# Optimization experiments

Measured on AMD Instinct MI355X. Metric: run time of the kernel, lower is better.

The kernel has to match this reference:

```python
import jax, jax.numpy as jnp
import numpy as np

B, C, E = 4, 2048, 1024
H, D = 16, 64


def setup_inputs() -> dict:
    key = jax.random.key(0)
    kx, kq, kk, kv, ko = jax.random.split(key, 5)
    s = 0.02
    return {
        "x": jax.random.normal(kx, (B, C, E), dtype=jnp.float32),
        "W_q": jax.random.normal(kq, (E, H * D), dtype=jnp.float32) * s,
        "W_k": jax.random.normal(kk, (E, H * D), dtype=jnp.float32) * s,
        "W_v": jax.random.normal(kv, (E, H * D), dtype=jnp.float32) * s,
        "W_o": jax.random.normal(ko, (H * D, E), dtype=jnp.float32) * s,
    }


def reference(x, W_q, W_k, W_v, W_o):
    b, c, e = x.shape
    # projections -> [B, H, C, D]
    def split_heads(t):
        return t.reshape(b, c, H, D).transpose(0, 2, 1, 3)
    Q = split_heads(x @ W_q)
    K = split_heads(x @ W_k)
    V = split_heads(x @ W_v)
    scale = 1.0 / jnp.sqrt(jnp.asarray(D, dtype=x.dtype))
    scores = jnp.einsum("bhqd,bhkd->bhqk", Q, K) * scale  # [B,H,C,C]
    causal = jnp.tril(jnp.ones((c, c), dtype=bool))
    scores = jnp.where(causal, scores, jnp.asarray(-jnp.inf, dtype=scores.dtype))
    weights = jax.nn.softmax(scores, axis=-1)
    hidden = jnp.einsum("bhqk,bhkd->bhqd", weights, V)  # [B,H,C,D]
    hidden = hidden.transpose(0, 2, 1, 3).reshape(b, c, H * D)
    return hidden @ W_o
```

## Files before the change

kernel.cpp:

```cpp
#include <hip/hip_runtime.h>

typedef __bf16 bf16;
typedef __attribute__((ext_vector_type(8))) __bf16 bf16x8;
typedef __attribute__((ext_vector_type(4))) __bf16 bf16x4;
typedef __attribute__((ext_vector_type(4))) float f32x4;
typedef __attribute__((ext_vector_type(16))) float f32x16;

#define B_ 4
#define C_ 2048
#define E_ 1024
#define H_ 16
#define D_ 64

__device__ __forceinline__ void gload16(const void* g, void* l) {
  __builtin_amdgcn_global_load_lds(
      (const __attribute__((address_space(1))) void*)g,
      (__attribute__((address_space(3))) void*)l, 16, 0, 0);
}

__device__ __forceinline__ unsigned cvtpk(float lo, float hi) {
  unsigned r;
  asm("v_cvt_pk_bf16_f32 %0, %1, %2" : "=v"(r) : "v"(lo), "v"(hi));
  return r;
}
__device__ __forceinline__ void pswap(unsigned& a, unsigned& b) {
  asm volatile("v_permlane32_swap_b32 %0, %1" : "+v"(a), "+v"(b));
}
__device__ __forceinline__ bf16x8 mkfrag(unsigned d0, unsigned d1, unsigned d2,
                                         unsigned d3) {
  union {
    unsigned u[4];
    bf16x8 v;
  } x;
  x.u[0] = d0;
  x.u[1] = d1;
  x.u[2] = d2;
  x.u[3] = d3;
  return x.v;
}

__global__ __launch_bounds__(256) void xconv(const float* __restrict__ x,
                                             bf16* __restrict__ xb) {
  const size_t i = (size_t)blockIdx.x * 256 + threadIdx.x;
  const float4* p = (const float4*)(x + i * 8);
  float4 a = p[0], b = p[1];
  bf16x8 v = {(__bf16)a.x, (__bf16)a.y, (__bf16)a.z, (__bf16)a.w,
              (__bf16)b.x, (__bf16)b.y, (__bf16)b.z, (__bf16)b.w};
  *(bf16x8*)(xb + i * 8) = v;
}

__global__ __launch_bounds__(256) void wtrans(const float* __restrict__ Wq,
                                              const float* __restrict__ Wk,
                                              const float* __restrict__ Wv,
                                              const float* __restrict__ Wo,
                                              bf16* __restrict__ WT) {
  const float* W = blockIdx.z == 0 ? Wq : blockIdx.z == 1 ? Wk
                 : blockIdx.z == 2 ? Wv : Wo;
  bf16* dst = WT + (size_t)blockIdx.z * 1024 * 1024;
  __shared__ bf16 t[64][65];
  const int tx = threadIdx.x & 63, ty = threadIdx.x >> 6;
  const int r0 = blockIdx.y * 64, c0 = blockIdx.x * 64;
#pragma unroll
  for (int r = ty; r < 64; r += 4)
    t[tx][r] = (__bf16)W[(size_t)(r0 + r) * 1024 + c0 + tx];
  __syncthreads();
#pragma unroll
  for (int r = ty; r < 64; r += 4)
    dst[(size_t)(c0 + r) * 1024 + r0 + tx] = t[r][tx];
}

template <int MODE>
__global__ __launch_bounds__(256, 2) void gemm_bt(const bf16* __restrict__ A,
                                                  const bf16* __restrict__ WTall,
                                                  bf16* __restrict__ Qo,
                                                  bf16* __restrict__ Ko,
                                                  bf16* __restrict__ Vto,
                                                  float* __restrict__ Fo) {
  constexpr int BK = 64;
  constexpr int NT = 1024 / BK;
  const int tid = threadIdx.x;
  const int wave = tid >> 6, lane = tid & 63;
  const int cl = lane & 15, g = lane >> 4;
  const int wr = wave >> 1, wc = wave & 1;
  const int brow = blockIdx.x * 128;
  const int bcol = blockIdx.y * 128;
  const bf16* Bt =
      (MODE == 0) ? (WTall + (size_t)blockIdx.z * 1024 * 1024) : WTall;

  __shared__ __align__(16) bf16 ldsA[2][128 * BK];
  __shared__ __align__(16) bf16 ldsB[2][128 * BK];

  f32x4 acc[4][4] = {};

  auto STAGE = [&](int kt, int buf) {
#pragma unroll
    for (int it = 0; it < 4; ++it) {
      const int chunk = it * 256 + tid;
      const int row = chunk >> 3, slot = chunk & 7;
      const int se = (slot ^ (row & 7)) * 8;
      const int ldsoff = (it * 256 + wave * 64) * 16;
      gload16(A + (size_t)(brow + row) * 1024 + kt + se,
              (char*)&ldsA[buf][0] + ldsoff);
      gload16(Bt + (size_t)(bcol + row) * 1024 + kt + se,
              (char*)&ldsB[buf][0] + ldsoff);
    }
  };

  STAGE(0, 0);
  STAGE(BK, 1);
  asm volatile("s_waitcnt vmcnt(8)" ::: "memory");
  __builtin_amdgcn_s_barrier();

  for (int t = 0; t < NT; ++t) {
    const int buf = t & 1;
    bf16x8 af[2][4], bfr[2][4];
#pragma unroll
    for (int kkid = 0; kkid < 2; ++kkid) {
#pragma unroll
      for (int i = 0; i < 4; ++i) {
        const int sl = ((4 * kkid + g) ^ (cl & 7)) * 8;
        af[kkid][i] = *(const bf16x8*)&ldsA[buf][(wr * 64 + i * 16 + cl) * BK + sl];
        bfr[kkid][i] = *(const bf16x8*)&ldsB[buf][(wc * 64 + i * 16 + cl) * BK + sl];
      }
    }
    asm volatile("s_waitcnt lgkmcnt(0)" ::: "memory");
    __builtin_amdgcn_sched_barrier(0);
    __builtin_amdgcn_s_barrier();

    if (t + 2 < NT) STAGE((t + 2) * BK, buf);

#pragma unroll
    for (int kkid = 0; kkid < 2; ++kkid)
#pragma unroll
      for (int i = 0; i < 4; ++i)
#pragma unroll
        for (int j = 0; j < 4; ++j)
          acc[i][j] = __builtin_amdgcn_mfma_f32_16x16x32_bf16(
              af[kkid][i], bfr[kkid][j], acc[i][j], 0, 0, 0);

    if (t + 2 < NT)
      asm volatile("s_waitcnt vmcnt(8)" ::: "memory");
    else
      asm volatile("s_waitcnt vmcnt(0)" ::: "memory");
    __builtin_amdgcn_s_barrier();
  }

  bf16* dst = nullptr;
  if constexpr (MODE == 0)
    dst = blockIdx.z == 0 ? Qo : blockIdx.z == 1 ? Ko : Vto;
  const float presc =
      (MODE == 0 && blockIdx.z == 0) ? 0.18033688011112042f : 1.0f;
#pragma unroll
  for (int i = 0; i < 4; ++i) {
#pragma unroll
    for (int j = 0; j < 4; ++j) {
#pragma unroll
      for (int r = 0; r < 4; ++r) {
        const int gr = brow + wr * 64 + i * 16 + g * 4 + r;
        const int gc = bcol + wc * 64 + j * 16 + cl;
        const float v = acc[i][j][r] * presc;
        if constexpr (MODE == 0) {
          const int b = gr >> 11, c = gr & 2047;
          const int h = gc >> 6, d = gc & 63;
          if (blockIdx.z == 2)
            dst[(((size_t)b * H_ + h) * D_ + d) * C_ + c] = (__bf16)v;
          else
            dst[(((size_t)b * H_ + h) * C_ + c) * D_ + d] = (__bf16)v;
        } else {
          Fo[(size_t)gr * 1024 + gc] = v;
        }
      }
    }
  }
}

__device__ __forceinline__ void sm_fixed(f32x16& s0, f32x16& s1, f32x4& l4,
                                         int th0, bool domask, int hi,
                                         bf16x8& pf0, bf16x8& pf1,
                                         bf16x8& pf2, bf16x8& pf3) {
  if (domask) {
#pragma unroll
    for (int r = 0; r < 16; ++r) {
      const int crow = (r & 3) + 8 * (r >> 2) + 4 * hi;
      if (crow > th0) s0[r] = -1e30f;
      if (crow + 32 > th0) s1[r] = -1e30f;
    }
  }
#pragma unroll
  for (int r = 0; r < 16; ++r) {
    s0[r] = __builtin_amdgcn_exp2f(s0[r]);
    s1[r] = __builtin_amdgcn_exp2f(s1[r]);
  }
#pragma unroll
  for (int r = 0; r < 16; ++r) l4[r & 3] += s0[r] + s1[r];
  unsigned a0 = cvtpk(s0[0], s0[1]), a1 = cvtpk(s0[2], s0[3]);
  unsigned b0 = cvtpk(s0[4], s0[5]), b1 = cvtpk(s0[6], s0[7]);
  unsigned c0 = cvtpk(s0[8], s0[9]), c1 = cvtpk(s0[10], s0[11]);
  unsigned d0 = cvtpk(s0[12], s0[13]), d1 = cvtpk(s0[14], s0[15]);
  unsigned e0 = cvtpk(s1[0], s1[1]), e1 = cvtpk(s1[2], s1[3]);
  unsigned f0 = cvtpk(s1[4], s1[5]), f1 = cvtpk(s1[6], s1[7]);
  unsigned g0 = cvtpk(s1[8], s1[9]), g1 = cvtpk(s1[10], s1[11]);
  unsigned h0 = cvtpk(s1[12], s1[13]), h1 = cvtpk(s1[14], s1[15]);
  pswap(a0, b0);
  pswap(a1, b1);
  pswap(c0, d0);
  pswap(c1, d1);
  pswap(e0, f0);
  pswap(e1, f1);
  pswap(g0, h0);
  pswap(g1, h1);
  pf0 = mkfrag(a0, a1, b0, b1);
  pf1 = mkfrag(c0, c1, d0, d1);
  pf2 = mkfrag(e0, e1, f0, f1);
  pf3 = mkfrag(g0, g1, h0, h1);
}

__global__ __launch_bounds__(256, 2) void attn(const bf16* __restrict__ Qg,
                                               const bf16* __restrict__ Kg,
                                               const bf16* __restrict__ Vt,
                                               bf16* __restrict__ Hid) {
  const int tid = threadIdx.x, wave = tid >> 6, lane = tid & 63;
  const int l31 = lane & 31, hi = lane >> 5, l7 = lane & 7;
  const int qa = blockIdx.x, qb = 15 - (int)blockIdx.x;
  const int h = blockIdx.y, b = blockIdx.z;
  const size_t bh = (size_t)b * H_ + h;

  __shared__ __align__(16) bf16 ldsK[2 * 64 * 64];
  __shared__ __align__(16) bf16 ldsV[2 * 64 * 64];

  const bf16* Kb = Kg + bh * C_ * D_;
  const bf16* Vb = Vt + bh * (size_t)D_ * C_;

  const int qrowA = qa * 128 + wave * 32;
  const int qrowB = qb * 128 + wave * 32;

  bf16x8 qfA[4], qfB[4];
  {
    const bf16* qra = Qg + (bh * C_ + qrowA + l31) * D_;
    const bf16* qrb = Qg + (bh * C_ + qrowB + l31) * D_;
#pragma unroll
    for (int ds = 0; ds < 4; ++ds) {
      qfA[ds] = *(const bf16x8*)(qra + ds * 16 + 8 * hi);
      qfB[ds] = *(const bf16x8*)(qrb + ds * 16 + 8 * hi);
    }
  }

  f32x4 l4A = {}, l4B = {};
  f32x16 oA0 = {}, oA1 = {}, oB0 = {}, oB1 = {};

  auto STAGE = [&](int kt, int buf) {
#pragma unroll
    for (int it = 0; it < 2; ++it) {
      const int chunk = it * 256 + tid;
      const int row = chunk >> 3, slot = chunk & 7;
      const int se = (slot ^ (row & 7)) * 8;
      const int ldsoff = buf * 8192 + (it * 256 + wave * 64) * 16;
      gload16(Kb + (size_t)kt * 64 * D_ + row * 64 + se, (char*)ldsK + ldsoff);
      gload16(Vb + (size_t)row * C_ + kt * 64 + se, (char*)ldsV + ldsoff);
    }
  };

  const int last = 2 * qb + 1;
  STAGE(0, 0);

  for (int kt = 0; kt <= last; ++kt) {
    const int cur = kt & 1;
    const bf16* kb = ldsK + cur * 4096;
    const bf16* vb = ldsV + cur * 4096;
    if (kt < last) {
      STAGE(kt + 1, cur ^ 1);
      asm volatile("s_waitcnt vmcnt(4)" ::: "memory");
    } else {
      asm volatile("s_waitcnt vmcnt(0)" ::: "memory");
    }
    __builtin_amdgcn_s_barrier();
    __builtin_amdgcn_sched_barrier(0);

    const bool actA = (kt * 64 <= qrowA + 31);
    const bool actB = (kt * 64 <= qrowB + 31);

    f32x16 sA0 = {}, sA1 = {}, sB0 = {}, sB1 = {};
    __builtin_amdgcn_s_setprio(1);
#pragma unroll
    for (int ds = 0; ds < 4; ++ds) {
      const int sl = ((2 * ds + hi) ^ l7) * 8;
      bf16x8 kf0 = *(const bf16x8*)&kb[l31 * 64 + sl];
      bf16x8 kf1 = *(const bf16x8*)&kb[(32 + l31) * 64 + sl];
      if (actA) {
        sA0 = __builtin_amdgcn_mfma_f32_32x32x16_bf16(kf0, qfA[ds], sA0, 0, 0, 0);
        sA1 = __builtin_amdgcn_mfma_f32_32x32x16_bf16(kf1, qfA[ds], sA1, 0, 0, 0);
      }
      if (actB) {
        sB0 = __builtin_amdgcn_mfma_f32_32x32x16_bf16(kf0, qfB[ds], sB0, 0, 0, 0);
        sB1 = __builtin_amdgcn_mfma_f32_32x32x16_bf16(kf1, qfB[ds], sB1, 0, 0, 0);
      }
    }
    __builtin_amdgcn_s_setprio(0);

    bf16x8 vf0[4], vf1[4];
#pragma unroll
    for (int ks = 0; ks < 4; ++ks) {
      const int sl = ((2 * ks + hi) ^ l7) * 8;
      vf0[ks] = *(const bf16x8*)&vb[l31 * 64 + sl];
      vf1[ks] = *(const bf16x8*)&vb[(32 + l31) * 64 + sl];
    }

    if (actA) {
      bf16x8 p0, p1, p2, p3;
      sm_fixed(sA0, sA1, l4A, qrowA + l31 - kt * 64, kt * 64 + 63 > qrowA, hi,
               p0, p1, p2, p3);
      __builtin_amdgcn_s_setprio(1);
      oA0 = __builtin_amdgcn_mfma_f32_32x32x16_bf16(vf0[0], p0, oA0, 0, 0, 0);
      oA1 = __builtin_amdgcn_mfma_f32_32x32x16_bf16(vf1[0], p0, oA1, 0, 0, 0);
      oA0 = __builtin_amdgcn_mfma_f32_32x32x16_bf16(vf0[1], p1, oA0, 0, 0, 0);
      oA1 = __builtin_amdgcn_mfma_f32_32x32x16_bf16(vf1[1], p1, oA1, 0, 0, 0);
      oA0 = __builtin_amdgcn_mfma_f32_32x32x16_bf16(vf0[2], p2, oA0, 0, 0, 0);
      oA1 = __builtin_amdgcn_mfma_f32_32x32x16_bf16(vf1[2], p2, oA1, 0, 0, 0);
      oA0 = __builtin_amdgcn_mfma_f32_32x32x16_bf16(vf0[3], p3, oA0, 0, 0, 0);
      oA1 = __builtin_amdgcn_mfma_f32_32x32x16_bf16(vf1[3], p3, oA1, 0, 0, 0);
      __builtin_amdgcn_s_setprio(0);
    }
    if (actB) {
      bf16x8 p0, p1, p2, p3;
      sm_fixed(sB0, sB1, l4B, qrowB + l31 - kt * 64, kt * 64 + 63 > qrowB, hi,
               p0, p1, p2, p3);
      __builtin_amdgcn_s_setprio(1);
      oB0 = __builtin_amdgcn_mfma_f32_32x32x16_bf16(vf0[0], p0, oB0, 0, 0, 0);
      oB1 = __builtin_amdgcn_mfma_f32_32x32x16_bf16(vf1[0], p0, oB1, 0, 0, 0);
      oB0 = __builtin_amdgcn_mfma_f32_32x32x16_bf16(vf0[1], p1, oB0, 0, 0, 0);
      oB1 = __builtin_amdgcn_mfma_f32_32x32x16_bf16(vf1[1], p1, oB1, 0, 0, 0);
      oB0 = __builtin_amdgcn_mfma_f32_32x32x16_bf16(vf0[2], p2, oB0, 0, 0, 0);
      oB1 = __builtin_amdgcn_mfma_f32_32x32x16_bf16(vf1[2], p2, oB1, 0, 0, 0);
      oB0 = __builtin_amdgcn_mfma_f32_32x32x16_bf16(vf0[3], p3, oB0, 0, 0, 0);
      oB1 = __builtin_amdgcn_mfma_f32_32x32x16_bf16(vf1[3], p3, oB1, 0, 0, 0);
      __builtin_amdgcn_s_setprio(0);
    }
    __builtin_amdgcn_s_barrier();
  }

#pragma unroll
  for (int st = 0; st < 2; ++st) {
    const f32x4 l4 = st ? l4B : l4A;
    float l = (l4[0] + l4[1]) + (l4[2] + l4[3]);
    l += __shfl_xor(l, 32, 64);
    const float inv = 1.0f / l;
    const int qrow = st ? qrowB : qrowA;
    const size_t row = (size_t)b * C_ + qrow + l31;
#pragma unroll
    for (int dt = 0; dt < 2; ++dt) {
      const f32x16& oo = st ? (dt ? oB1 : oB0) : (dt ? oA1 : oA0);
#pragma unroll
      for (int q4 = 0; q4 < 4; ++q4) {
        bf16x4 pk = {(__bf16)(oo[4 * q4 + 0] * inv),
                     (__bf16)(oo[4 * q4 + 1] * inv),
                     (__bf16)(oo[4 * q4 + 2] * inv),
                     (__bf16)(oo[4 * q4 + 3] * inv)};
        const int d = dt * 32 + 8 * q4 + 4 * hi;
        *(bf16x4*)&Hid[row * (H_ * D_) + h * 64 + d] = pk;
      }
    }
  }
}

extern "C" void kernel_launch(void* const* d_in, const int* in_sizes, int n_in,
                              void* d_out, int out_size, void* d_ws,
                              size_t ws_size, hipStream_t stream) {
  const float* x = (const float*)d_in[0];
  const float* Wq = (const float*)d_in[1];
  const float* Wk = (const float*)d_in[2];
  const float* Wv = (const float*)d_in[3];
  const float* Wo = (const float*)d_in[4];

  char* ws = (char*)d_ws;
  bf16* xb = (bf16*)ws;
  bf16* WT = (bf16*)(ws + (16ull << 20));
  bf16* Qb = (bf16*)(ws + (24ull << 20));
  bf16* Kb = (bf16*)(ws + (40ull << 20));
  bf16* Vtb = (bf16*)(ws + (56ull << 20));
  bf16* Hid = (bf16*)(ws + (72ull << 20));

  xconv<<<dim3(4096), 256, 0, stream>>>(x, xb);
  wtrans<<<dim3(16, 16, 4), 256, 0, stream>>>(Wq, Wk, Wv, Wo, WT);
  gemm_bt<0><<<dim3(64, 8, 3), 256, 0, stream>>>(xb, WT, Qb, Kb, Vtb, nullptr);
  attn<<<dim3(8, H_, B_), 256, 0, stream>>>(Qb, Kb, Vtb, Hid);
  gemm_bt<1><<<dim3(64, 8, 1), 256, 0, stream>>>(
      Hid, WT + 3ull * 1024 * 1024, nullptr, nullptr, nullptr, (float*)d_out);
}
```

Baseline: 160.4 us.

## Fuse x fp32-to-bf16 conversion into QKV GEMM and widen attention KV tiles

Removes the separate xconv kernel: the QKV projection GEMM now loads fp32 x into registers, converts it to bf16 with packed converts, and writes it swizzled into LDS, with the waitcnt pipeline restructured around this. It also raises MFMA priority around the GEMM compute loop. The attention kernel stages 128-key K/V tiles per iteration, processed as two 64-key halves, which halves the number of barriers and staging rounds but doubles LDS use. The GEMM reads twice as many bytes of x per tile and relies on register staging instead of direct global-to-LDS loads, and the larger attention LDS footprint may lower occupancy.

```diff
diff --git a/kernel.cpp b/kernel.cpp
--- a/kernel.cpp
+++ b/kernel.cpp
@@ -39,16 +39,6 @@
   return x.v;
 }
 
-__global__ __launch_bounds__(256) void xconv(const float* __restrict__ x,
-                                             bf16* __restrict__ xb) {
-  const size_t i = (size_t)blockIdx.x * 256 + threadIdx.x;
-  const float4* p = (const float4*)(x + i * 8);
-  float4 a = p[0], b = p[1];
-  bf16x8 v = {(__bf16)a.x, (__bf16)a.y, (__bf16)a.z, (__bf16)a.w,
-              (__bf16)b.x, (__bf16)b.y, (__bf16)b.z, (__bf16)b.w};
-  *(bf16x8*)(xb + i * 8) = v;
-}
-
 __global__ __launch_bounds__(256) void wtrans(const float* __restrict__ Wq,
                                               const float* __restrict__ Wk,
                                               const float* __restrict__ Wv,
@@ -70,7 +60,8 @@
 }
 
 template <int MODE>
-__global__ __launch_bounds__(256, 2) void gemm_bt(const bf16* __restrict__ A,
+__global__ __launch_bounds__(256, 2) void gemm_bt(const float* __restrict__ X,
+                                                  const bf16* __restrict__ Ahid,
                                                   const bf16* __restrict__ WTall,
                                                   bf16* __restrict__ Qo,
                                                   bf16* __restrict__ Ko,
@@ -91,25 +82,70 @@
   __shared__ __align__(16) bf16 ldsB[2][128 * BK];
 
   f32x4 acc[4][4] = {};
-
-  auto STAGE = [&](int kt, int buf) {
+  float4 ar[8];
+
+  auto ISSUE_B = [&](int kt, int buf) {
 #pragma unroll
     for (int it = 0; it < 4; ++it) {
       const int chunk = it * 256 + tid;
       const int row = chunk >> 3, slot = chunk & 7;
       const int se = (slot ^ (row & 7)) * 8;
-      const int ldsoff = (it * 256 + wave * 64) * 16;
-      gload16(A + (size_t)(brow + row) * 1024 + kt + se,
-              (char*)&ldsA[buf][0] + ldsoff);
       gload16(Bt + (size_t)(bcol + row) * 1024 + kt + se,
-              (char*)&ldsB[buf][0] + ldsoff);
+              (char*)&ldsB[buf][0] + (it * 256 + wave * 64) * 16);
     }
   };
-
-  STAGE(0, 0);
-  STAGE(BK, 1);
-  asm volatile("s_waitcnt vmcnt(8)" ::: "memory");
-  __builtin_amdgcn_s_barrier();
+  auto ISSUE_A = [&](int kt, int buf) {
+    if constexpr (MODE == 0) {
+#pragma unroll
+      for (int w = 0; w < 4; ++w) {
+        const int chunk = w * 256 + tid;
+        const int row = chunk >> 3, slot = chunk & 7;
+        const float* src = X + (size_t)(brow + row) * 1024 + kt + slot * 8;
+        ar[2 * w] = *(const float4*)(src);
+        ar[2 * w + 1] = *(const float4*)(src + 4);
+      }
+    } else {
+#pragma unroll
+      for (int it = 0; it < 4; ++it) {
+        const int chunk = it * 256 + tid;
+        const int row = chunk >> 3, slot = chunk & 7;
+        const int se = (slot ^ (row & 7)) * 8;
+        gload16(Ahid + (size_t)(brow + row) * 1024 + kt + se,
+                (char*)&ldsA[buf][0] + (it * 256 + wave * 64) * 16);
+      }
+    }
+  };
+  auto WRITE_A = [&](int buf) {
+#pragma unroll
+    for (int w = 0; w < 4; ++w) {
+      const int chunk = w * 256 + tid;
+      const int row = chunk >> 3, slot = chunk & 7;
+      const unsigned p0 = cvtpk(ar[2 * w].x, ar[2 * w].y);
+      const unsigned p1 = cvtpk(ar[2 * w].z, ar[2 * w].w);
+      const unsigned p2 = cvtpk(ar[2 * w + 1].x, ar[2 * w + 1].y);
+      const unsigned p3 = cvtpk(ar[2 * w + 1].z, ar[2 * w + 1].w);
+      *(bf16x8*)((char*)&ldsA[buf][0] + row * 128 + ((slot ^ (row & 7)) * 16)) =
+          mkfrag(p0, p1, p2, p3);
+    }
+  };
+
+  if constexpr (MODE == 0) {
+    ISSUE_A(0, 0);
+    ISSUE_B(0, 0);
+    asm volatile("s_waitcnt vmcnt(0)" ::: "memory");
+    WRITE_A(0);
+    ISSUE_A(BK, 1);
+    ISSUE_B(BK, 1);
+    asm volatile("s_waitcnt lgkmcnt(0)" ::: "memory");
+    __builtin_amdgcn_s_barrier();
+  } else {
+    ISSUE_A(0, 0);
+    ISSUE_B(0, 0);
+    ISSUE_A(BK, 1);
+    ISSUE_B(BK, 1);
+    asm volatile("s_waitcnt vmcnt(8)" ::: "memory");
+    __builtin_amdgcn_s_barrier();
+  }
 
   for (int t = 0; t < NT; ++t) {
     const int buf = t & 1;
@@ -127,8 +163,24 @@
     __builtin_amdgcn_sched_barrier(0);
     __builtin_amdgcn_s_barrier();
 
-    if (t + 2 < NT) STAGE((t + 2) * BK, buf);
-
+    if constexpr (MODE == 0) {
+      if (t + 1 < NT) {
+        asm volatile("s_waitcnt vmcnt(4)" ::: "memory");
+        WRITE_A(buf ^ 1);
+      }
+      if (t + 2 < NT) {
+        ISSUE_A((t + 2) * BK, buf);
+        ISSUE_B((t + 2) * BK, buf);
+      }
+      __builtin_amdgcn_sched_barrier(0);
+    } else {
+      if (t + 2 < NT) {
+        ISSUE_A((t + 2) * BK, buf);
+        ISSUE_B((t + 2) * BK, buf);
+      }
+    }
+
+    __builtin_amdgcn_s_setprio(1);
 #pragma unroll
     for (int kkid = 0; kkid < 2; ++kkid)
 #pragma unroll
@@ -137,11 +189,21 @@
         for (int j = 0; j < 4; ++j)
           acc[i][j] = __builtin_amdgcn_mfma_f32_16x16x32_bf16(
               af[kkid][i], bfr[kkid][j], acc[i][j], 0, 0, 0);
-
-    if (t + 2 < NT)
-      asm volatile("s_waitcnt vmcnt(8)" ::: "memory");
-    else
-      asm volatile("s_waitcnt vmcnt(0)" ::: "memory");
+    __builtin_amdgcn_s_setprio(0);
+
+    if constexpr (MODE == 0) {
+      if (t + 2 < NT)
+        asm volatile("s_waitcnt vmcnt(12)" ::: "memory");
+      else if (t + 1 < NT)
+        asm volatile("s_waitcnt vmcnt(0)" ::: "memory");
+      if (t + 1 < NT)
+        asm volatile("s_waitcnt lgkmcnt(0)" ::: "memory");
+    } else {
+      if (t + 2 < NT)
+        asm volatile("s_waitcnt vmcnt(8)" ::: "memory");
+      else
+        asm volatile("s_waitcnt vmcnt(0)" ::: "memory");
+    }
     __builtin_amdgcn_s_barrier();
   }
 
@@ -225,8 +287,8 @@
   const int h = blockIdx.y, b = blockIdx.z;
   const size_t bh = (size_t)b * H_ + h;
 
-  __shared__ __align__(16) bf16 ldsK[2 * 64 * 64];
-  __shared__ __align__(16) bf16 ldsV[2 * 64 * 64];
+  __shared__ __align__(16) bf16 ldsK[2 * 128 * 64];
+  __shared__ __align__(16) bf16 ldsV[2 * 64 * 128];
 
   const bf16* Kb = Kg + bh * C_ * D_;
   const bf16* Vb = Vt + bh * (size_t)D_ * C_;
@@ -250,90 +312,102 @@
 
   auto STAGE = [&](int kt, int buf) {
 #pragma unroll
-    for (int it = 0; it < 2; ++it) {
-      const int chunk = it * 256 + tid;
-      const int row = chunk >> 3, slot = chunk & 7;
-      const int se = (slot ^ (row & 7)) * 8;
-      const int ldsoff = buf * 8192 + (it * 256 + wave * 64) * 16;
-      gload16(Kb + (size_t)kt * 64 * D_ + row * 64 + se, (char*)ldsK + ldsoff);
-      gload16(Vb + (size_t)row * C_ + kt * 64 + se, (char*)ldsV + ldsoff);
+    for (int w = 0; w < 4; ++w) {
+      const int chunk = w * 256 + tid;
+      {
+        const int row = chunk >> 3, slot = chunk & 7;
+        const int se = (slot ^ (row & 7)) * 8;
+        gload16(Kb + ((size_t)kt * 128 + row) * D_ + se,
+                (char*)ldsK + buf * 16384 + (w * 256 + wave * 64) * 16);
+      }
+      {
+        const int row = chunk >> 4, slot = chunk & 15;
+        const int se = (slot ^ (row & 7)) * 8;
+        gload16(Vb + (size_t)row * C_ + kt * 128 + se,
+                (char*)ldsV + buf * 16384 + (w * 256 + wave * 64) * 16);
+      }
     }
   };
 
-  const int last = 2 * qb + 1;
+  const int nkv = qb + 1;
   STAGE(0, 0);
 
-  for (int kt = 0; kt <= last; ++kt) {
+  for (int kt = 0; kt < nkv; ++kt) {
     const int cur = kt & 1;
-    const bf16* kb = ldsK + cur * 4096;
-    const bf16* vb = ldsV + cur * 4096;
-    if (kt < last) {
+    const bf16* kb = ldsK + cur * 8192;
+    const bf16* vb = ldsV + cur * 8192;
+    if (kt + 1 < nkv) {
       STAGE(kt + 1, cur ^ 1);
-      asm volatile("s_waitcnt vmcnt(4)" ::: "memory");
+      asm volatile("s_waitcnt vmcnt(8)" ::: "memory");
     } else {
       asm volatile("s_waitcnt vmcnt(0)" ::: "memory");
     }
     __builtin_amdgcn_s_barrier();
     __builtin_amdgcn_sched_barrier(0);
 
-    const bool actA = (kt * 64 <= qrowA + 31);
-    const bool actB = (kt * 64 <= qrowB + 31);
-
-    f32x16 sA0 = {}, sA1 = {}, sB0 = {}, sB1 = {};
-    __builtin_amdgcn_s_setprio(1);
-#pragma unroll
-    for (int ds = 0; ds < 4; ++ds) {
-      const int sl = ((2 * ds + hi) ^ l7) * 8;
-      bf16x8 kf0 = *(const bf16x8*)&kb[l31 * 64 + sl];
-      bf16x8 kf1 = *(const bf16x8*)&kb[(32 + l31) * 64 + sl];
+#pragma unroll
+    for (int hh = 0; hh < 2; ++hh) {
+      const int key0 = kt * 128 + hh * 64;
+      const bool actA = (key0 <= qrowA + 31);
+      const bool actB = (key0 <= qrowB + 31);
+      if (!actA && !actB) continue;
+
+      f32x16 sA0 = {}, sA1 = {}, sB0 = {}, sB1 = {};
+      __builtin_amdgcn_s_setprio(1);
+#pragma unroll
+      for (int ds = 0; ds < 4; ++ds) {
+        const int r0 = hh * 64 + l31, r1 = hh * 64 + 32 + l31;
+        bf16x8 kf0 = *(const bf16x8*)&kb[r0 * 64 + (((2 * ds + hi) ^ (r0 & 7)) * 8)];
+        bf16x8 kf1 = *(const bf16x8*)&kb[r1 * 64 + (((2 * ds + hi) ^ (r1 & 7)) * 8)];
+        if (actA) {
+          sA0 = __builtin_amdgcn_mfma_f32_32x32x16_bf16(kf0, qfA[ds], sA0, 0, 0, 0);
+          sA1 = __builtin_amdgcn_mfma_f32_32x32x16_bf16(kf1, qfA[ds], sA1, 0, 0, 0);
+        }
+        if (actB) {
+          sB0 = __builtin_amdgcn_mfma_f32_32x32x16_bf16(kf0, qfB[ds], sB0, 0, 0, 0);
+          sB1 = __builtin_amdgcn_mfma_f32_32x32x16_bf16(kf1, qfB[ds], sB1, 0, 0, 0);
+        }
+      }
+      __builtin_amdgcn_s_setprio(0);
+
+      bf16x8 vf0[4], vf1[4];
+#pragma unroll
+      for (int ks = 0; ks < 4; ++ks) {
+        const int gs = hh * 8 + 2 * ks + hi;
+        vf0[ks] = *(const bf16x8*)&vb[l31 * 128 + ((gs ^ (l31 & 7)) * 8)];
+        vf1[ks] = *(const bf16x8*)&vb[(32 + l31) * 128 + ((gs ^ ((32 + l31) & 7)) * 8)];
+      }
+
       if (actA) {
-        sA0 = __builtin_amdgcn_mfma_f32_32x32x16_bf16(kf0, qfA[ds], sA0, 0, 0, 0);
-        sA1 = __builtin_amdgcn_mfma_f32_32x32x16_bf16(kf1, qfA[ds], sA1, 0, 0, 0);
+        bf16x8 p0, p1, p2, p3;
+        sm_fixed(sA0, sA1, l4A, qrowA + l31 - key0, key0 + 63 > qrowA, hi,
+                 p0, p1, p2, p3);
+        __builtin_amdgcn_s_setprio(1);
+        oA0 = __builtin_amdgcn_mfma_f32_32x32x16_bf16(vf0[0], p0, oA0, 0, 0, 0);
+        oA1 = __builtin_amdgcn_mfma_f32_32x32x16_bf16(vf1[0], p0, oA1, 0, 0, 0);
+        oA0 = __builtin_amdgcn_mfma_f32_32x32x16_bf16(vf0[1], p1, oA0, 0, 0, 0);
+        oA1 = __builtin_amdgcn_mfma_f32_32x32x16_bf16(vf1[1], p1, oA1, 0, 0, 0);
+        oA0 = __builtin_amdgcn_mfma_f32_32x32x16_bf16(vf0[2], p2, oA0, 0, 0, 0);
+        oA1 = __builtin_amdgcn_mfma_f32_32x32x16_bf16(vf1[2], p2, oA1, 0, 0, 0);
+        oA0 = __builtin_amdgcn_mfma_f32_32x32x16_bf16(vf0[3], p3, oA0, 0, 0, 0);
+        oA1 = __builtin_amdgcn_mfma_f32_32x32x16_bf16(vf1[3], p3, oA1, 0, 0, 0);
+        __builtin_amdgcn_s_setprio(0);
       }
       if (actB) {
-        sB0 = __builtin_amdgcn_mfma_f32_32x32x16_bf16(kf0, qfB[ds], sB0, 0, 0, 0);
-        sB1 = __builtin_amdgcn_mfma_f32_32x32x16_bf16(kf1, qfB[ds], sB1, 0, 0, 0);
-      }
-    }
-    __builtin_amdgcn_s_setprio(0);
-
-    bf16x8 vf0[4], vf1[4];
-#pragma unroll
-    for (int ks = 0; ks < 4; ++ks) {
-      const int sl = ((2 * ks + hi) ^ l7) * 8;
-      vf0[ks] = *(const bf16x8*)&vb[l31 * 64 + sl];
-      vf1[ks] = *(const bf16x8*)&vb[(32 + l31) * 64 + sl];
-    }
-
-    if (actA) {
-      bf16x8 p0, p1, p2, p3;
-      sm_fixed(sA0, sA1, l4A, qrowA + l31 - kt * 64, kt * 64 + 63 > qrowA, hi,
-               p0, p1, p2, p3);
-      __builtin_amdgcn_s_setprio(1);
-      oA0 = __builtin_amdgcn_mfma_f32_32x32x16_bf16(vf0[0], p0, oA0, 0, 0, 0);
-      oA1 = __builtin_amdgcn_mfma_f32_32x32x16_bf16(vf1[0], p0, oA1, 0, 0, 0);
-      oA0 = __builtin_amdgcn_mfma_f32_32x32x16_bf16(vf0[1], p1, oA0, 0, 0, 0);
-      oA1 = __builtin_amdgcn_mfma_f32_32x32x16_bf16(vf1[1], p1, oA1, 0, 0, 0);
-      oA0 = __builtin_amdgcn_mfma_f32_32x32x16_bf16(vf0[2], p2, oA0, 0, 0, 0);
-      oA1 = __builtin_amdgcn_mfma_f32_32x32x16_bf16(vf1[2], p2, oA1, 0, 0, 0);
-      oA0 = __builtin_amdgcn_mfma_f32_32x32x16_bf16(vf0[3], p3, oA0, 0, 0, 0);
-      oA1 = __builtin_amdgcn_mfma_f32_32x32x16_bf16(vf1[3], p3, oA1, 0, 0, 0);
-      __builtin_amdgcn_s_setprio(0);
-    }
-    if (actB) {
-      bf16x8 p0, p1, p2, p3;
-      sm_fixed(sB0, sB1, l4B, qrowB + l31 - kt * 64, kt * 64 + 63 > qrowB, hi,
-               p0, p1, p2, p3);
-      __builtin_amdgcn_s_setprio(1);
-      oB0 = __builtin_amdgcn_mfma_f32_32x32x16_bf16(vf0[0], p0, oB0, 0, 0, 0);
-      oB1 = __builtin_amdgcn_mfma_f32_32x32x16_bf16(vf1[0], p0, oB1, 0, 0, 0);
-      oB0 = __builtin_amdgcn_mfma_f32_32x32x16_bf16(vf0[1], p1, oB0, 0, 0, 0);
-      oB1 = __builtin_amdgcn_mfma_f32_32x32x16_bf16(vf1[1], p1, oB1, 0, 0, 0);
-      oB0 = __builtin_amdgcn_mfma_f32_32x32x16_bf16(vf0[2], p2, oB0, 0, 0, 0);
-      oB1 = __builtin_amdgcn_mfma_f32_32x32x16_bf16(vf1[2], p2, oB1, 0, 0, 0);
-      oB0 = __builtin_amdgcn_mfma_f32_32x32x16_bf16(vf0[3], p3, oB0, 0, 0, 0);
-      oB1 = __builtin_amdgcn_mfma_f32_32x32x16_bf16(vf1[3], p3, oB1, 0, 0, 0);
-      __builtin_amdgcn_s_setprio(0);
+        bf16x8 p0, p1, p2, p3;
+        sm_fixed(sB0, sB1, l4B, qrowB + l31 - key0, key0 + 63 > qrowB, hi,
+                 p0, p1, p2, p3);
+        __builtin_amdgcn_s_setprio(1);
+        oB0 = __builtin_amdgcn_mfma_f32_32x32x16_bf16(vf0[0], p0, oB0, 0, 0, 0);
+        oB1 = __builtin_amdgcn_mfma_f32_32x32x16_bf16(vf1[0], p0, oB1, 0, 0, 0);
+        oB0 = __builtin_amdgcn_mfma_f32_32x32x16_bf16(vf0[1], p1, oB0, 0, 0, 0);
+        oB1 = __builtin_amdgcn_mfma_f32_32x32x16_bf16(vf1[1], p1, oB1, 0, 0, 0);
+        oB0 = __builtin_amdgcn_mfma_f32_32x32x16_bf16(vf0[2], p2, oB0, 0, 0, 0);
+        oB1 = __builtin_amdgcn_mfma_f32_32x32x16_bf16(vf1[2], p2, oB1, 0, 0, 0);
+        oB0 = __builtin_amdgcn_mfma_f32_32x32x16_bf16(vf0[3], p3, oB0, 0, 0, 0);
+        oB1 = __builtin_amdgcn_mfma_f32_32x32x16_bf16(vf1[3], p3, oB1, 0, 0, 0);
+        __builtin_amdgcn_s_setprio(0);
+      }
     }
     __builtin_amdgcn_s_barrier();
   }
@@ -372,17 +446,17 @@
   const float* Wo = (const float*)d_in[4];
 
   char* ws = (char*)d_ws;
-  bf16* xb = (bf16*)ws;
   bf16* WT = (bf16*)(ws + (16ull << 20));
   bf16* Qb = (bf16*)(ws + (24ull << 20));
   bf16* Kb = (bf16*)(ws + (40ull << 20));
   bf16* Vtb = (bf16*)(ws + (56ull << 20));
   bf16* Hid = (bf16*)(ws + (72ull << 20));
 
-  xconv<<<dim3(4096), 256, 0, stream>>>(x, xb);
   wtrans<<<dim3(16, 16, 4), 256, 0, stream>>>(Wq, Wk, Wv, Wo, WT);
-  gemm_bt<0><<<dim3(64, 8, 3), 256, 0, stream>>>(xb, WT, Qb, Kb, Vtb, nullptr);
+  gemm_bt<0><<<dim3(64, 8, 3), 256, 0, stream>>>(x, nullptr, WT, Qb, Kb, Vtb,
+                                                 nullptr);
   attn<<<dim3(8, H_, B_), 256, 0, stream>>>(Qb, Kb, Vtb, Hid);
   gemm_bt<1><<<dim3(64, 8, 1), 256, 0, stream>>>(
-      Hid, WT + 3ull * 1024 * 1024, nullptr, nullptr, nullptr, (float*)d_out);
-}
+      nullptr, Hid, WT + 3ull * 1024 * 1024, nullptr, nullptr, nullptr,
+      (float*)d_out);
+}
```

New measurement: 178.0 us. 11.0% more time.

## Use 256x256 8-wave QKV GEMM and 128-key attention staging tiles

Applied to the files above, without the earlier changes.

Replaces the QKV projection GEMM with a 512-thread, 256x256-tile kernel. It uses a phased ping-pong LDS pipeline that interleaves loads of A and B halves with MFMA phases, raising arithmetic intensity per staged byte. The attention kernel now stages 128 keys per iteration, processed as two 64-key halves, which halves the number of barriers and load waits per KV sweep. The output GEMM is split into its own simplified kernel. The trade-offs are more LDS use and more registers per block, which may lower occupancy, and the 256-tile GEMM launches only 384 blocks.

```diff
diff --git a/kernel.cpp b/kernel.cpp
--- a/kernel.cpp
+++ b/kernel.cpp
@@ -69,13 +69,140 @@
     dst[(size_t)(c0 + r) * 1024 + r0 + tx] = t[r][tx];
 }
 
-template <int MODE>
-__global__ __launch_bounds__(256, 2) void gemm_bt(const bf16* __restrict__ A,
-                                                  const bf16* __restrict__ WTall,
-                                                  bf16* __restrict__ Qo,
-                                                  bf16* __restrict__ Ko,
-                                                  bf16* __restrict__ Vto,
-                                                  float* __restrict__ Fo) {
+__global__ __launch_bounds__(512, 2) void gemm8(const bf16* __restrict__ A,
+                                                const bf16* __restrict__ WTall,
+                                                bf16* __restrict__ Qo,
+                                                bf16* __restrict__ Ko,
+                                                bf16* __restrict__ Vto) {
+  const int tid = threadIdx.x;
+  const int wave = tid >> 6, lane = tid & 63;
+  const int cl = lane & 15, g = lane >> 4;
+  const int wm = wave >> 2, wn = wave & 3;
+  const int brow = blockIdx.x * 256;
+  const int bcol = blockIdx.y * 256;
+  const bf16* Bt = WTall + (size_t)blockIdx.z * 1024 * 1024;
+
+  __shared__ __align__(16) bf16 lA[2][2][128 * 64];
+  __shared__ __align__(16) bf16 lB[2][2][128 * 64];
+
+  f32x4 acc[8][4] = {};
+  bf16x8 bfr[2][4];
+
+  auto STA = [&](int kt, int h) {
+    const int d = kt & 1;
+#pragma unroll
+    for (int it = 0; it < 2; ++it) {
+      const int chunk = it * 512 + tid;
+      const int row = chunk >> 3, slot = chunk & 7;
+      const int se = (slot ^ (row & 7)) * 8;
+      gload16(A + (size_t)(brow + h * 128 + row) * 1024 + kt * 64 + se,
+              (char*)&lA[d][h][0] + (it * 512 + wave * 64) * 16);
+    }
+  };
+  auto STB = [&](int kt, int h) {
+    const int d = kt & 1;
+#pragma unroll
+    for (int it = 0; it < 2; ++it) {
+      const int chunk = it * 512 + tid;
+      const int row = chunk >> 3, slot = chunk & 7;
+      const int se = (slot ^ (row & 7)) * 8;
+      gload16(Bt + (size_t)(bcol + h * 128 + row) * 1024 + kt * 64 + se,
+              (char*)&lB[d][h][0] + (it * 512 + wave * 64) * 16);
+    }
+  };
+
+#define RA_(d, i, kk)                                                       \
+  (*(const bf16x8*)&lA[d][wm][(i * 16 + cl) * 64 +                          \
+                              (((4 * kk + g) ^ ((i * 16 + cl) & 7)) * 8)])
+#define RB_(d, j, kk)                                                        \
+  (*(const bf16x8*)&lB[d][wn >> 1][((wn & 1) * 64 + j * 16 + cl) * 64 +      \
+                                   (((4 * kk + g) ^                          \
+                                     (((wn & 1) * 64 + j * 16 + cl) & 7)) *  \
+                                    8)])
+
+#define PHASE(d, q, STG, WAITC)                                              \
+  {                                                                          \
+    bf16x8 af00 = RA_(d, (2 * (q)), 0), af01 = RA_(d, (2 * (q) + 1), 0);     \
+    bf16x8 af10 = RA_(d, (2 * (q)), 1), af11 = RA_(d, (2 * (q) + 1), 1);     \
+    if ((q) == 0) {                                                          \
+      bfr[0][0] = RB_(d, 0, 0); bfr[0][1] = RB_(d, 1, 0);                    \
+      bfr[0][2] = RB_(d, 2, 0); bfr[0][3] = RB_(d, 3, 0);                    \
+      bfr[1][0] = RB_(d, 0, 1); bfr[1][1] = RB_(d, 1, 1);                    \
+      bfr[1][2] = RB_(d, 2, 1); bfr[1][3] = RB_(d, 3, 1);                    \
+    }                                                                        \
+    STG;                                                                     \
+    __builtin_amdgcn_s_barrier();                                            \
+    asm volatile("s_waitcnt lgkmcnt(0)" ::: "memory");                       \
+    __builtin_amdgcn_sched_barrier(0);                                       \
+    __builtin_amdgcn_s_setprio(1);                                           \
+    _Pragma("unroll") for (int j = 0; j < 4; ++j) {                          \
+      acc[2 * (q)][j] = __builtin_amdgcn_mfma_f32_16x16x32_bf16(             \
+          af00, bfr[0][j], acc[2 * (q)][j], 0, 0, 0);                        \
+      acc[2 * (q) + 1][j] = __builtin_amdgcn_mfma_f32_16x16x32_bf16(         \
+          af01, bfr[0][j], acc[2 * (q) + 1][j], 0, 0, 0);                    \
+    }                                                                        \
+    _Pragma("unroll") for (int j = 0; j < 4; ++j) {                          \
+      acc[2 * (q)][j] = __builtin_amdgcn_mfma_f32_16x16x32_bf16(             \
+          af10, bfr[1][j], acc[2 * (q)][j], 0, 0, 0);                        \
+      acc[2 * (q) + 1][j] = __builtin_amdgcn_mfma_f32_16x16x32_bf16(         \
+          af11, bfr[1][j], acc[2 * (q) + 1][j], 0, 0, 0);                    \
+    }                                                                        \
+    __builtin_amdgcn_s_setprio(0);                                           \
+    WAITC;                                                                   \
+    __builtin_amdgcn_s_barrier();                                            \
+  }
+
+  STA(0, 0); STA(0, 1); STB(0, 0); STB(0, 1); STB(1, 0); STB(1, 1);
+  asm volatile("s_waitcnt vmcnt(4)" ::: "memory");
+  __builtin_amdgcn_s_barrier();
+
+  for (int t = 0; t < 8; ++t) {
+    const int k1 = 2 * t + 1;
+    const bool li = (t == 7);
+    PHASE(0, 0, STA(k1, 0), );
+    PHASE(0, 1, STA(k1, 1), );
+    PHASE(0, 2, if (!li) STB(k1 + 1, 0), );
+    PHASE(0, 3, if (!li) STB(k1 + 1, 1), {
+      if (li) { asm volatile("s_waitcnt vmcnt(0)" ::: "memory"); }
+      else    { asm volatile("s_waitcnt vmcnt(4)" ::: "memory"); }
+    });
+    PHASE(1, 0, if (!li) STA(k1 + 1, 0), );
+    PHASE(1, 1, if (!li) STA(k1 + 1, 1), );
+    PHASE(1, 2, if (!li) STB(k1 + 2, 0), );
+    PHASE(1, 3, if (!li) STB(k1 + 2, 1), {
+      if (li) { asm volatile("s_waitcnt vmcnt(0)" ::: "memory"); }
+      else    { asm volatile("s_waitcnt vmcnt(4)" ::: "memory"); }
+    });
+  }
+#undef PHASE
+#undef RA_
+#undef RB_
+
+  bf16* dst = blockIdx.z == 0 ? Qo : blockIdx.z == 1 ? Ko : Vto;
+  const float presc = (blockIdx.z == 0) ? 0.18033688011112042f : 1.0f;
+#pragma unroll
+  for (int i = 0; i < 8; ++i) {
+#pragma unroll
+    for (int j = 0; j < 4; ++j) {
+#pragma unroll
+      for (int r = 0; r < 4; ++r) {
+        const int gr = brow + wm * 128 + i * 16 + g * 4 + r;
+        const int gc = bcol + wn * 64 + j * 16 + cl;
+        const float v = acc[i][j][r] * presc;
+        const int b = gr >> 11, c = gr & 2047;
+        const int hh = gc >> 6, dd = gc & 63;
+        if (blockIdx.z == 2)
+          dst[(((size_t)b * H_ + hh) * D_ + dd) * C_ + c] = (__bf16)v;
+        else
+          dst[(((size_t)b * H_ + hh) * C_ + c) * D_ + dd] = (__bf16)v;
+      }
+    }
+  }
+}
+
+__global__ __launch_bounds__(256, 2) void gemm_o(const bf16* __restrict__ A,
+                                                 const bf16* __restrict__ Bt,
+                                                 float* __restrict__ Fo) {
   constexpr int BK = 64;
   constexpr int NT = 1024 / BK;
   const int tid = threadIdx.x;
@@ -84,8 +211,6 @@
   const int wr = wave >> 1, wc = wave & 1;
   const int brow = blockIdx.x * 128;
   const int bcol = blockIdx.y * 128;
-  const bf16* Bt =
-      (MODE == 0) ? (WTall + (size_t)blockIdx.z * 1024 * 1024) : WTall;
 
   __shared__ __align__(16) bf16 ldsA[2][128 * BK];
   __shared__ __align__(16) bf16 ldsB[2][128 * BK];
@@ -145,33 +270,16 @@
     __builtin_amdgcn_s_barrier();
   }
 
-  bf16* dst = nullptr;
-  if constexpr (MODE == 0)
-    dst = blockIdx.z == 0 ? Qo : blockIdx.z == 1 ? Ko : Vto;
-  const float presc =
-      (MODE == 0 && blockIdx.z == 0) ? 0.18033688011112042f : 1.0f;
-#pragma unroll
-  for (int i = 0; i < 4; ++i) {
-#pragma unroll
-    for (int j = 0; j < 4; ++j) {
+#pragma unroll
+  for (int i = 0; i < 4; ++i)
+#pragma unroll
+    for (int j = 0; j < 4; ++j)
 #pragma unroll
       for (int r = 0; r < 4; ++r) {
         const int gr = brow + wr * 64 + i * 16 + g * 4 + r;
         const int gc = bcol + wc * 64 + j * 16 + cl;
-        const float v = acc[i][j][r] * presc;
-        if constexpr (MODE == 0) {
-          const int b = gr >> 11, c = gr & 2047;
-          const int h = gc >> 6, d = gc & 63;
-          if (blockIdx.z == 2)
-            dst[(((size_t)b * H_ + h) * D_ + d) * C_ + c] = (__bf16)v;
-          else
-            dst[(((size_t)b * H_ + h) * C_ + c) * D_ + d] = (__bf16)v;
-        } else {
-          Fo[(size_t)gr * 1024 + gc] = v;
-        }
-      }
-    }
-  }
+        Fo[(size_t)gr * 1024 + gc] = acc[i][j][r];
+      }
 }
 
 __device__ __forceinline__ void sm_fixed(f32x16& s0, f32x16& s1, f32x4& l4,
@@ -225,8 +333,8 @@
   const int h = blockIdx.y, b = blockIdx.z;
   const size_t bh = (size_t)b * H_ + h;
 
-  __shared__ __align__(16) bf16 ldsK[2 * 64 * 64];
-  __shared__ __align__(16) bf16 ldsV[2 * 64 * 64];
+  __shared__ __align__(16) bf16 ldsK[2 * 128 * 64];
+  __shared__ __align__(16) bf16 ldsV[2 * 64 * 128];
 
   const bf16* Kb = Kg + bh * C_ * D_;
   const bf16* Vb = Vt + bh * (size_t)D_ * C_;
@@ -250,90 +358,102 @@
 
   auto STAGE = [&](int kt, int buf) {
 #pragma unroll
-    for (int it = 0; it < 2; ++it) {
-      const int chunk = it * 256 + tid;
-      const int row = chunk >> 3, slot = chunk & 7;
-      const int se = (slot ^ (row & 7)) * 8;
-      const int ldsoff = buf * 8192 + (it * 256 + wave * 64) * 16;
-      gload16(Kb + (size_t)kt * 64 * D_ + row * 64 + se, (char*)ldsK + ldsoff);
-      gload16(Vb + (size_t)row * C_ + kt * 64 + se, (char*)ldsV + ldsoff);
+    for (int w = 0; w < 4; ++w) {
+      const int chunk = w * 256 + tid;
+      {
+        const int row = chunk >> 3, slot = chunk & 7;
+        const int se = (slot ^ (row & 7)) * 8;
+        gload16(Kb + ((size_t)kt * 128 + row) * D_ + se,
+                (char*)ldsK + buf * 16384 + (w * 256 + wave * 64) * 16);
+      }
+      {
+        const int row = chunk >> 4, slot = chunk & 15;
+        const int se = (slot ^ (row & 7)) * 8;
+        gload16(Vb + (size_t)row * C_ + kt * 128 + se,
+                (char*)ldsV + buf * 16384 + (w * 256 + wave * 64) * 16);
+      }
     }
   };
 
-  const int last = 2 * qb + 1;
+  const int nkv = qb + 1;
   STAGE(0, 0);
 
-  for (int kt = 0; kt <= last; ++kt) {
+  for (int kt = 0; kt < nkv; ++kt) {
     const int cur = kt & 1;
-    const bf16* kb = ldsK + cur * 4096;
-    const bf16* vb = ldsV + cur * 4096;
-    if (kt < last) {
+    const bf16* kb = ldsK + cur * 8192;
+    const bf16* vb = ldsV + cur * 8192;
+    if (kt + 1 < nkv) {
       STAGE(kt + 1, cur ^ 1);
-      asm volatile("s_waitcnt vmcnt(4)" ::: "memory");
+      asm volatile("s_waitcnt vmcnt(8)" ::: "memory");
     } else {
       asm volatile("s_waitcnt vmcnt(0)" ::: "memory");
     }
     __builtin_amdgcn_s_barrier();
     __builtin_amdgcn_sched_barrier(0);
 
-    const bool actA = (kt * 64 <= qrowA + 31);
-    const bool actB = (kt * 64 <= qrowB + 31);
-
-    f32x16 sA0 = {}, sA1 = {}, sB0 = {}, sB1 = {};
-    __builtin_amdgcn_s_setprio(1);
-#pragma unroll
-    for (int ds = 0; ds < 4; ++ds) {
-      const int sl = ((2 * ds + hi) ^ l7) * 8;
-      bf16x8 kf0 = *(const bf16x8*)&kb[l31 * 64 + sl];
-      bf16x8 kf1 = *(const bf16x8*)&kb[(32 + l31) * 64 + sl];
+#pragma unroll
+    for (int hh = 0; hh < 2; ++hh) {
+      const int key0 = kt * 128 + hh * 64;
+      const bool actA = (key0 <= qrowA + 31);
+      const bool actB = (key0 <= qrowB + 31);
+      if (!actA && !actB) continue;
+
+      f32x16 sA0 = {}, sA1 = {}, sB0 = {}, sB1 = {};
+      __builtin_amdgcn_s_setprio(1);
+#pragma unroll
+      for (int ds = 0; ds < 4; ++ds) {
+        const int r0 = hh * 64 + l31, r1 = hh * 64 + 32 + l31;
+        bf16x8 kf0 = *(const bf16x8*)&kb[r0 * 64 + (((2 * ds + hi) ^ (r0 & 7)) * 8)];
+        bf16x8 kf1 = *(const bf16x8*)&kb[r1 * 64 + (((2 * ds + hi) ^ (r1 & 7)) * 8)];
+        if (actA) {
+          sA0 = __builtin_amdgcn_mfma_f32_32x32x16_bf16(kf0, qfA[ds], sA0, 0, 0, 0);
+          sA1 = __builtin_amdgcn_mfma_f32_32x32x16_bf16(kf1, qfA[ds], sA1, 0, 0, 0);
+        }
+        if (actB) {
+          sB0 = __builtin_amdgcn_mfma_f32_32x32x16_bf16(kf0, qfB[ds], sB0, 0, 0, 0);
+          sB1 = __builtin_amdgcn_mfma_f32_32x32x16_bf16(kf1, qfB[ds], sB1, 0, 0, 0);
+        }
+      }
+      __builtin_amdgcn_s_setprio(0);
+
+      bf16x8 vf0[4], vf1[4];
+#pragma unroll
+      for (int ks = 0; ks < 4; ++ks) {
+        const int gs = hh * 8 + 2 * ks + hi;
+        vf0[ks] = *(const bf16x8*)&vb[l31 * 128 + ((gs ^ (l31 & 7)) * 8)];
+        vf1[ks] = *(const bf16x8*)&vb[(32 + l31) * 128 + ((gs ^ ((32 + l31) & 7)) * 8)];
+      }
+
       if (actA) {
-        sA0 = __builtin_amdgcn_mfma_f32_32x32x16_bf16(kf0, qfA[ds], sA0, 0, 0, 0);
-        sA1 = __builtin_amdgcn_mfma_f32_32x32x16_bf16(kf1, qfA[ds], sA1, 0, 0, 0);
+        bf16x8 p0, p1, p2, p3;
+        sm_fixed(sA0, sA1, l4A, qrowA + l31 - key0, key0 + 63 > qrowA, hi,
+                 p0, p1, p2, p3);
+        __builtin_amdgcn_s_setprio(1);
+        oA0 = __builtin_amdgcn_mfma_f32_32x32x16_bf16(vf0[0], p0, oA0, 0, 0, 0);
+        oA1 = __builtin_amdgcn_mfma_f32_32x32x16_bf16(vf1[0], p0, oA1, 0, 0, 0);
+        oA0 = __builtin_amdgcn_mfma_f32_32x32x16_bf16(vf0[1], p1, oA0, 0, 0, 0);
+        oA1 = __builtin_amdgcn_mfma_f32_32x32x16_bf16(vf1[1], p1, oA1, 0, 0, 0);
+        oA0 = __builtin_amdgcn_mfma_f32_32x32x16_bf16(vf0[2], p2, oA0, 0, 0, 0);
+        oA1 = __builtin_amdgcn_mfma_f32_32x32x16_bf16(vf1[2], p2, oA1, 0, 0, 0);
+        oA0 = __builtin_amdgcn_mfma_f32_32x32x16_bf16(vf0[3], p3, oA0, 0, 0, 0);
+        oA1 = __builtin_amdgcn_mfma_f32_32x32x16_bf16(vf1[3], p3, oA1, 0, 0, 0);
+        __builtin_amdgcn_s_setprio(0);
       }
       if (actB) {
-        sB0 = __builtin_amdgcn_mfma_f32_32x32x16_bf16(kf0, qfB[ds], sB0, 0, 0, 0);
-        sB1 = __builtin_amdgcn_mfma_f32_32x32x16_bf16(kf1, qfB[ds], sB1, 0, 0, 0);
-      }
-    }
-    __builtin_amdgcn_s_setprio(0);
-
-    bf16x8 vf0[4], vf1[4];
-#pragma unroll
-    for (int ks = 0; ks < 4; ++ks) {
-      const int sl = ((2 * ks + hi) ^ l7) * 8;
-      vf0[ks] = *(const bf16x8*)&vb[l31 * 64 + sl];
-      vf1[ks] = *(const bf16x8*)&vb[(32 + l31) * 64 + sl];
-    }
-
-    if (actA) {
-      bf16x8 p0, p1, p2, p3;
-      sm_fixed(sA0, sA1, l4A, qrowA + l31 - kt * 64, kt * 64 + 63 > qrowA, hi,
-               p0, p1, p2, p3);
-      __builtin_amdgcn_s_setprio(1);
-      oA0 = __builtin_amdgcn_mfma_f32_32x32x16_bf16(vf0[0], p0, oA0, 0, 0, 0);
-      oA1 = __builtin_amdgcn_mfma_f32_32x32x16_bf16(vf1[0], p0, oA1, 0, 0, 0);
-      oA0 = __builtin_amdgcn_mfma_f32_32x32x16_bf16(vf0[1], p1, oA0, 0, 0, 0);
-      oA1 = __builtin_amdgcn_mfma_f32_32x32x16_bf16(vf1[1], p1, oA1, 0, 0, 0);
-      oA0 = __builtin_amdgcn_mfma_f32_32x32x16_bf16(vf0[2], p2, oA0, 0, 0, 0);
-      oA1 = __builtin_amdgcn_mfma_f32_32x32x16_bf16(vf1[2], p2, oA1, 0, 0, 0);
-      oA0 = __builtin_amdgcn_mfma_f32_32x32x16_bf16(vf0[3], p3, oA0, 0, 0, 0);
-      oA1 = __builtin_amdgcn_mfma_f32_32x32x16_bf16(vf1[3], p3, oA1, 0, 0, 0);
-      __builtin_amdgcn_s_setprio(0);
-    }
-    if (actB) {
-      bf16x8 p0, p1, p2, p3;
-      sm_fixed(sB0, sB1, l4B, qrowB + l31 - kt * 64, kt * 64 + 63 > qrowB, hi,
-               p0, p1, p2, p3);
-      __builtin_amdgcn_s_setprio(1);
-      oB0 = __builtin_amdgcn_mfma_f32_32x32x16_bf16(vf0[0], p0, oB0, 0, 0, 0);
-      oB1 = __builtin_amdgcn_mfma_f32_32x32x16_bf16(vf1[0], p0, oB1, 0, 0, 0);
-      oB0 = __builtin_amdgcn_mfma_f32_32x32x16_bf16(vf0[1], p1, oB0, 0, 0, 0);
-      oB1 = __builtin_amdgcn_mfma_f32_32x32x16_bf16(vf1[1], p1, oB1, 0, 0, 0);
-      oB0 = __builtin_amdgcn_mfma_f32_32x32x16_bf16(vf0[2], p2, oB0, 0, 0, 0);
-      oB1 = __builtin_amdgcn_mfma_f32_32x32x16_bf16(vf1[2], p2, oB1, 0, 0, 0);
-      oB0 = __builtin_amdgcn_mfma_f32_32x32x16_bf16(vf0[3], p3, oB0, 0, 0, 0);
-      oB1 = __builtin_amdgcn_mfma_f32_32x32x16_bf16(vf1[3], p3, oB1, 0, 0, 0);
-      __builtin_amdgcn_s_setprio(0);
+        bf16x8 p0, p1, p2, p3;
+        sm_fixed(sB0, sB1, l4B, qrowB + l31 - key0, key0 + 63 > qrowB, hi,
+                 p0, p1, p2, p3);
+        __builtin_amdgcn_s_setprio(1);
+        oB0 = __builtin_amdgcn_mfma_f32_32x32x16_bf16(vf0[0], p0, oB0, 0, 0, 0);
+        oB1 = __builtin_amdgcn_mfma_f32_32x32x16_bf16(vf1[0], p0, oB1, 0, 0, 0);
+        oB0 = __builtin_amdgcn_mfma_f32_32x32x16_bf16(vf0[1], p1, oB0, 0, 0, 0);
+        oB1 = __builtin_amdgcn_mfma_f32_32x32x16_bf16(vf1[1], p1, oB1, 0, 0, 0);
+        oB0 = __builtin_amdgcn_mfma_f32_32x32x16_bf16(vf0[2], p2, oB0, 0, 0, 0);
+        oB1 = __builtin_amdgcn_mfma_f32_32x32x16_bf16(vf1[2], p2, oB1, 0, 0, 0);
+        oB0 = __builtin_amdgcn_mfma_f32_32x32x16_bf16(vf0[3], p3, oB0, 0, 0, 0);
+        oB1 = __builtin_amdgcn_mfma_f32_32x32x16_bf16(vf1[3], p3, oB1, 0, 0, 0);
+        __builtin_amdgcn_s_setprio(0);
+      }
     }
     __builtin_amdgcn_s_barrier();
   }
@@ -381,8 +501,8 @@
 
   xconv<<<dim3(4096), 256, 0, stream>>>(x, xb);
   wtrans<<<dim3(16, 16, 4), 256, 0, stream>>>(Wq, Wk, Wv, Wo, WT);
-  gemm_bt<0><<<dim3(64, 8, 3), 256, 0, stream>>>(xb, WT, Qb, Kb, Vtb, nullptr);
+  gemm8<<<dim3(32, 4, 3), 512, 0, stream>>>(xb, WT, Qb, Kb, Vtb);
   attn<<<dim3(8, H_, B_), 256, 0, stream>>>(Qb, Kb, Vtb, Hid);
-  gemm_bt<1><<<dim3(64, 8, 1), 256, 0, stream>>>(
-      Hid, WT + 3ull * 1024 * 1024, nullptr, nullptr, nullptr, (float*)d_out);
-}
+  gemm_o<<<dim3(64, 8), 256, 0, stream>>>(Hid, WT + 3ull * 1024 * 1024,
+                                          (float*)d_out);
+}
```

Measured after the change: 183.5 us. +14.4%, slower.
